# Kernel tuning notes

Measured on AMD Instinct MI355X. Metric: run time of the kernel, lower is better.

The kernel has to match this reference:

```python
import jax, jax.numpy as jnp
import numpy as np

PADDING_IDX = 0


def setup_inputs() -> dict:
    key = jax.random.key(0)
    k1, k2 = jax.random.split(key)
    B, S, D = 64, 2048, 128
    V = 200000
    grad_output = jax.random.normal(k1, (B, S, D), dtype=jnp.float32)
    indices = jax.random.randint(k2, (B, S), 0, V, dtype=jnp.int64)
    return {"grad_output": grad_output, "indices": indices, "num_embeddings": V}


def reference(grad_output, indices, num_embeddings):
    D = grad_output.shape[-1]
    flat_idx = indices.reshape(-1)                      # [B*S]
    flat_grad = grad_output.reshape(-1, D)              # [B*S, D]
    # Zero out contributions from padding positions; padding row stays 0,
    # matching the original (it never accumulates into padding_idx).
    mask = (flat_idx != PADDING_IDX)[:, None]           # [B*S, 1]
    masked_grad = jnp.where(mask, flat_grad, jnp.zeros((), dtype=flat_grad.dtype))
    dense_grad = jax.ops.segment_sum(masked_grad, flat_idx,
                                     num_segments=num_embeddings)
    return dense_grad.astype(jnp.float32)
```

## Files before the change

kernel.cpp:

```cpp
#include <hip/hip_runtime.h>


#define EMB_D   128
#define PAD_IDX 0
#define MAXC    8
#define OVF_CAP 16384

typedef float fvec4 __attribute__((ext_vector_type(4)));

__global__ void __launch_bounds__(256)
scatter_slots(const int* __restrict__ idx, unsigned* __restrict__ counts,
              unsigned* __restrict__ slots, unsigned* __restrict__ ovfcnt,
              uint2* __restrict__ ovf, int n) {
    int i = blockIdx.x * blockDim.x + threadIdx.x;
    if (i >= n) return;
    int e = idx[i];
    if (e == PAD_IDX) return;
    unsigned p = atomicAdd(&counts[e], 1u);
    if (p < MAXC) {
        __builtin_nontemporal_store((unsigned)i, &slots[(size_t)e * MAXC + p]);
    } else {
        unsigned q = atomicAdd(ovfcnt, 1u);
        if (q < OVF_CAP) ovf[q] = make_uint2((unsigned)e, (unsigned)i);
    }
}

__global__ void __launch_bounds__(256)
reduce_write(const float* __restrict__ grad, const unsigned* __restrict__ counts,
             const uint4* __restrict__ slots4, const unsigned* __restrict__ ovfcnt,
             const uint2* __restrict__ ovf, float* __restrict__ out, int V) {
    int wid  = (blockIdx.x * 256 + (int)threadIdx.x) >> 6;
    int half = (threadIdx.x >> 5) & 1;
    int lane = threadIdx.x & 31;
    int v = wid * 2 + half;
    if (v >= V) return;

    const float4* __restrict__ g4 = (const float4*)grad;
    float4 acc = make_float4(0.f, 0.f, 0.f, 0.f);

    unsigned c = counts[v];
    if (c != 0u) {
        uint4 s0 = slots4[(size_t)v * 2];
        unsigned i1 = (c > 1u) ? s0.y : s0.x;
        unsigned i2 = (c > 2u) ? s0.z : s0.x;
        unsigned i3 = (c > 3u) ? s0.w : s0.x;
        float4 a0 = g4[(size_t)s0.x * 32 + lane];
        float4 a1 = g4[(size_t)i1   * 32 + lane];
        float4 a2 = g4[(size_t)i2   * 32 + lane];
        float4 a3 = g4[(size_t)i3   * 32 + lane];
        float m1 = (c > 1u) ? 1.f : 0.f;
        float m2 = (c > 2u) ? 1.f : 0.f;
        float m3 = (c > 3u) ? 1.f : 0.f;
        acc.x = a0.x + m1 * a1.x + m2 * a2.x + m3 * a3.x;
        acc.y = a0.y + m1 * a1.y + m2 * a2.y + m3 * a3.y;
        acc.z = a0.z + m1 * a1.z + m2 * a2.z + m3 * a3.z;
        acc.w = a0.w + m1 * a1.w + m2 * a2.w + m3 * a3.w;

        if (c > 4u) {
            uint4 s1 = slots4[(size_t)v * 2 + 1];
            unsigned j1 = (c > 5u) ? s1.y : s1.x;
            unsigned j2 = (c > 6u) ? s1.z : s1.x;
            unsigned j3 = (c > 7u) ? s1.w : s1.x;
            float4 b0 = g4[(size_t)s1.x * 32 + lane];
            float4 b1 = g4[(size_t)j1   * 32 + lane];
            float4 b2 = g4[(size_t)j2   * 32 + lane];
            float4 b3 = g4[(size_t)j3   * 32 + lane];
            float n1 = (c > 5u) ? 1.f : 0.f;
            float n2 = (c > 6u) ? 1.f : 0.f;
            float n3 = (c > 7u) ? 1.f : 0.f;
            acc.x += b0.x + n1 * b1.x + n2 * b2.x + n3 * b3.x;
            acc.y += b0.y + n1 * b1.y + n2 * b2.y + n3 * b3.y;
            acc.z += b0.z + n1 * b1.z + n2 * b2.z + n3 * b3.z;
            acc.w += b0.w + n1 * b1.w + n2 * b2.w + n3 * b3.w;

            if (c > (unsigned)MAXC) {
                unsigned n = *ovfcnt;
                if (n > OVF_CAP) n = OVF_CAP;
                for (unsigned q = 0; q < n; ++q) {
                    uint2 eo = ovf[q];
                    if (eo.x == (unsigned)v) {
                        float4 g = g4[(size_t)eo.y * 32 + lane];
                        acc.x += g.x; acc.y += g.y; acc.z += g.z; acc.w += g.w;
                    }
                }
            }
        }
    }
    fvec4 accv = { acc.x, acc.y, acc.z, acc.w };
    __builtin_nontemporal_store(accv, &((fvec4*)out)[(size_t)v * 32 + lane]);
}

__global__ void zero_f32x4(float4* __restrict__ p, long n4) {
    long i = (long)blockIdx.x * blockDim.x + threadIdx.x;
    long stride = (long)gridDim.x * blockDim.x;
    const float4 z = make_float4(0.f, 0.f, 0.f, 0.f);
    for (; i < n4; i += stride) p[i] = z;
}

__global__ void __launch_bounds__(256)
scatter_add_kernel(const float* __restrict__ grad, const int* __restrict__ idx,
                   float* __restrict__ out, int ntok) {
    int gid = blockIdx.x * blockDim.x + threadIdx.x;
    int token = gid >> 5;
    int d4 = gid & 31;
    if (token >= ntok) return;
    int e = idx[token];
    if (e == PAD_IDX) return;
    const float4 g = ((const float4*)grad)[(size_t)token * 32 + d4];
    float* dst = out + (size_t)e * EMB_D + d4 * 4;
    unsafeAtomicAdd(dst + 0, g.x);
    unsafeAtomicAdd(dst + 1, g.y);
    unsafeAtomicAdd(dst + 2, g.z);
    unsafeAtomicAdd(dst + 3, g.w);
}

extern "C" void kernel_launch(void* const* d_in, const int* in_sizes, int n_in,
                              void* d_out, int out_size, void* d_ws, size_t ws_size,
                              hipStream_t stream) {
    const float* grad = (const float*)d_in[0];
    const int*   idx  = (const int*)d_in[1];
    float*       out  = (float*)d_out;
    const int ntok = in_sizes[1];
    const int V = out_size / EMB_D;

    size_t off_counts = 0;
    size_t off_ovfcnt = off_counts + (size_t)V * 4;
    size_t off_slots  = off_ovfcnt + 16;
    size_t off_ovf    = off_slots + (size_t)V * MAXC * 4;
    size_t need       = off_ovf + (size_t)OVF_CAP * 8;

    if (ws_size < need) {
        zero_f32x4<<<4096, 256, 0, stream>>>((float4*)out, (long)out_size / 4);
        const int threads = ntok * 32;
        scatter_add_kernel<<<(threads + 255) / 256, 256, 0, stream>>>(grad, idx, out, ntok);
        return;
    }

    char* ws = (char*)d_ws;
    unsigned* counts = (unsigned*)(ws + off_counts);
    unsigned* ovfcnt = (unsigned*)(ws + off_ovfcnt);
    unsigned* slots  = (unsigned*)(ws + off_slots);
    uint2*    ovf    = (uint2*)(ws + off_ovf);

    (void)hipMemsetAsync(counts, 0, (size_t)V * 4 + 16, stream);

    scatter_slots<<<(ntok + 255) / 256, 256, 0, stream>>>(
        idx, counts, slots, ovfcnt, ovf, ntok);

    int waves = (V + 1) / 2;
    int nblocks = (waves + 3) / 4;
    reduce_write<<<nblocks, 256, 0, stream>>>(
        grad, counts, (const uint4*)slots, ovfcnt, ovf, out, V);
}
```

Measured before the change: 182.2 us.

## Process four embedding rows per half-wave to batch gathers for memory-level parallelism

Result: faster. 177.4 us (-2.6%).

```diff
diff --git a/kernel.cpp b/kernel.cpp
--- a/kernel.cpp
+++ b/kernel.cpp
@@ -18,7 +18,7 @@
     if (e == PAD_IDX) return;
     unsigned p = atomicAdd(&counts[e], 1u);
     if (p < MAXC) {
-        __builtin_nontemporal_store((unsigned)i, &slots[(size_t)e * MAXC + p]);
+        slots[(size_t)e * MAXC + p] = (unsigned)i;
     } else {
         unsigned q = atomicAdd(ovfcnt, 1u);
         if (q < OVF_CAP) ovf[q] = make_uint2((unsigned)e, (unsigned)i);
@@ -32,31 +32,63 @@
     int wid  = (blockIdx.x * 256 + (int)threadIdx.x) >> 6;
     int half = (threadIdx.x >> 5) & 1;
     int lane = threadIdx.x & 31;
-    int v = wid * 2 + half;
-    if (v >= V) return;
+    const float4* __restrict__ g4 = (const float4*)grad;
 
-    const float4* __restrict__ g4 = (const float4*)grad;
-    float4 acc = make_float4(0.f, 0.f, 0.f, 0.f);
+    int base = wid * 8;
+    if (base >= V) return;
 
-    unsigned c = counts[v];
-    if (c != 0u) {
-        uint4 s0 = slots4[(size_t)v * 2];
-        unsigned i1 = (c > 1u) ? s0.y : s0.x;
-        unsigned i2 = (c > 2u) ? s0.z : s0.x;
-        unsigned i3 = (c > 3u) ? s0.w : s0.x;
-        float4 a0 = g4[(size_t)s0.x * 32 + lane];
-        float4 a1 = g4[(size_t)i1   * 32 + lane];
-        float4 a2 = g4[(size_t)i2   * 32 + lane];
-        float4 a3 = g4[(size_t)i3   * 32 + lane];
-        float m1 = (c > 1u) ? 1.f : 0.f;
-        float m2 = (c > 2u) ? 1.f : 0.f;
-        float m3 = (c > 3u) ? 1.f : 0.f;
-        acc.x = a0.x + m1 * a1.x + m2 * a2.x + m3 * a3.x;
-        acc.y = a0.y + m1 * a1.y + m2 * a2.y + m3 * a3.y;
-        acc.z = a0.z + m1 * a1.z + m2 * a2.z + m3 * a3.z;
-        acc.w = a0.w + m1 * a1.w + m2 * a2.w + m3 * a3.w;
+    int      vr[4];
+    unsigned cs[4];
+    uint4    s0[4];
+    #pragma unroll
+    for (int p = 0; p < 4; ++p) {
+        int v = base + 2 * p + half;
+        int vc = v < V ? v : V - 1;
+        vr[p] = v;
+        cs[p] = counts[vc];
+        s0[p] = slots4[(size_t)vc * 2];
+    }
 
+    unsigned ia[4][4];
+    float    msk[4][3];
+    #pragma unroll
+    for (int p = 0; p < 4; ++p) {
+        unsigned c = cs[p];
+        if (vr[p] >= V || vr[p] == PAD_IDX) c = 0u;
+        cs[p] = c;
+        uint4 s = s0[p];
+        unsigned i0 = (c > 0u) ? s.x : 0u;
+        ia[p][0] = i0;
+        ia[p][1] = (c > 1u) ? s.y : i0;
+        ia[p][2] = (c > 2u) ? s.z : i0;
+        ia[p][3] = (c > 3u) ? s.w : i0;
+        msk[p][0] = (c > 1u) ? 1.f : 0.f;
+        msk[p][1] = (c > 2u) ? 1.f : 0.f;
+        msk[p][2] = (c > 3u) ? 1.f : 0.f;
+    }
+    float4 g[4][4];
+    #pragma unroll
+    for (int p = 0; p < 4; ++p)
+        #pragma unroll
+        for (int k = 0; k < 4; ++k)
+            g[p][k] = g4[(size_t)ia[p][k] * 32 + lane];
+
+    float4 acc[4];
+    #pragma unroll
+    for (int p = 0; p < 4; ++p) {
+        float z  = (cs[p] > 0u) ? 1.f : 0.f;
+        float m1 = msk[p][0], m2 = msk[p][1], m3 = msk[p][2];
+        acc[p].x = z * g[p][0].x + m1 * g[p][1].x + m2 * g[p][2].x + m3 * g[p][3].x;
+        acc[p].y = z * g[p][0].y + m1 * g[p][1].y + m2 * g[p][2].y + m3 * g[p][3].y;
+        acc[p].z = z * g[p][0].z + m1 * g[p][1].z + m2 * g[p][2].z + m3 * g[p][3].z;
+        acc[p].w = z * g[p][0].w + m1 * g[p][1].w + m2 * g[p][2].w + m3 * g[p][3].w;
+    }
+
+    #pragma unroll
+    for (int p = 0; p < 4; ++p) {
+        unsigned c = cs[p];
         if (c > 4u) {
+            int v = vr[p];
             uint4 s1 = slots4[(size_t)v * 2 + 1];
             unsigned j1 = (c > 5u) ? s1.y : s1.x;
             unsigned j2 = (c > 6u) ? s1.z : s1.x;
@@ -68,26 +100,32 @@
             float n1 = (c > 5u) ? 1.f : 0.f;
             float n2 = (c > 6u) ? 1.f : 0.f;
             float n3 = (c > 7u) ? 1.f : 0.f;
-            acc.x += b0.x + n1 * b1.x + n2 * b2.x + n3 * b3.x;
-            acc.y += b0.y + n1 * b1.y + n2 * b2.y + n3 * b3.y;
-            acc.z += b0.z + n1 * b1.z + n2 * b2.z + n3 * b3.z;
-            acc.w += b0.w + n1 * b1.w + n2 * b2.w + n3 * b3.w;
-
+            acc[p].x += b0.x + n1 * b1.x + n2 * b2.x + n3 * b3.x;
+            acc[p].y += b0.y + n1 * b1.y + n2 * b2.y + n3 * b3.y;
+            acc[p].z += b0.z + n1 * b1.z + n2 * b2.z + n3 * b3.z;
+            acc[p].w += b0.w + n1 * b1.w + n2 * b2.w + n3 * b3.w;
             if (c > (unsigned)MAXC) {
                 unsigned n = *ovfcnt;
                 if (n > OVF_CAP) n = OVF_CAP;
                 for (unsigned q = 0; q < n; ++q) {
                     uint2 eo = ovf[q];
                     if (eo.x == (unsigned)v) {
-                        float4 g = g4[(size_t)eo.y * 32 + lane];
-                        acc.x += g.x; acc.y += g.y; acc.z += g.z; acc.w += g.w;
+                        float4 gg = g4[(size_t)eo.y * 32 + lane];
+                        acc[p].x += gg.x; acc[p].y += gg.y;
+                        acc[p].z += gg.z; acc[p].w += gg.w;
                     }
                 }
             }
         }
     }
-    fvec4 accv = { acc.x, acc.y, acc.z, acc.w };
-    __builtin_nontemporal_store(accv, &((fvec4*)out)[(size_t)v * 32 + lane]);
+
+    #pragma unroll
+    for (int p = 0; p < 4; ++p) {
+        if (vr[p] < V) {
+            fvec4 av = { acc[p].x, acc[p].y, acc[p].z, acc[p].w };
+            __builtin_nontemporal_store(av, &((fvec4*)out)[(size_t)vr[p] * 32 + lane]);
+        }
+    }
 }
 
 __global__ void zero_f32x4(float4* __restrict__ p, long n4) {
@@ -147,7 +185,7 @@
     scatter_slots<<<(ntok + 255) / 256, 256, 0, stream>>>(
         idx, counts, slots, ovfcnt, ovf, ntok);
 
-    int waves = (V + 1) / 2;
+    int waves   = (V + 7) / 8;
     int nblocks = (waves + 3) / 4;
     reduce_write<<<nblocks, 256, 0, stream>>>(
         grad, counts, (const uint4*)slots, ovfcnt, ovf, out, V);
```
